# Performance work log

Hardware: AMD Instinct MI355X
Metric: run time of the kernel (lower is better)

The kernel has to match this reference:

```python
import jax, jax.numpy as jnp
import numpy as np

N_BALLS = 256
BATCH = 128
N_STEPS = 100
MAX_EVENTS = 5
WORLD_W = 10.0
WORLD_H = 10.0
RADIUS = 0.1
HID = 64
DT = 0.05
INF = jnp.float32(1e30)

_II_np, _JJ_np = np.triu_indices(N_BALLS, 1)
_II = jnp.asarray(_II_np)
_JJ = jnp.asarray(_JJ_np)
# wall order: left, right, bottom, top (normals point into the box)
_WN = jnp.array([[1.0, 0.0], [-1.0, 0.0], [0.0, 1.0], [0.0, -1.0]], dtype=jnp.float32)
_WP = jnp.array([0.0, -WORLD_W, 0.0, -WORLD_H], dtype=jnp.float32)


def setup_inputs():
    key = jax.random.key(0)
    ks = jax.random.split(key, 6)
    pos = jax.random.uniform(ks[0], (BATCH, N_BALLS, 2), minval=0.5, maxval=9.5)
    vel = jax.random.normal(ks[1], (BATCH, N_BALLS, 2))
    state = jnp.concatenate([pos, vel], axis=-1)  # [B, N, 4]
    radii = jnp.full((N_BALLS,), RADIUS, dtype=jnp.float32)
    sc = 0.1
    W1 = jax.random.normal(ks[2], (HID, 2)) * sc
    b1 = jnp.zeros((HID,), jnp.float32)
    W2 = jax.random.normal(ks[3], (HID, HID)) * sc
    b2 = jnp.zeros((HID,), jnp.float32)
    W3 = jax.random.normal(ks[4], (1, HID)) * sc
    b3 = jnp.zeros((1,), jnp.float32)
    return {"state": state, "radii": radii, "W1": W1, "b1": b1, "W2": W2,
            "b2": b2, "W3": W3, "b3": b3, "dt": DT, "n_steps": N_STEPS}


def _detect(pos, vel, radii):
    # pos, vel: [N,2]; vectorized replacement of the Python O(N^2) loop.
    diff = pos[_JJ] - pos[_II]                       # [P,2]
    dist = jnp.linalg.norm(diff, axis=-1)            # [P]
    gap_b = dist - (radii[_II] + radii[_JJ])
    nhat = diff / (dist + 1e-8)[:, None]
    app_b = jnp.sum((vel[_JJ] - vel[_II]) * nhat, axis=-1)
    gb = jnp.where(app_b < 0, gap_b, INF)            # only approaching pairs
    r = radii
    gw = jnp.stack([pos[:, 0] - r, WORLD_W - pos[:, 0] - r,
                    pos[:, 1] - r, WORLD_H - pos[:, 1] - r], axis=-1)  # [N,4]
    vw = jnp.stack([vel[:, 0] < 0, vel[:, 0] > 0,
                    vel[:, 1] < 0, vel[:, 1] > 0], axis=-1)
    gw = jnp.where(vw, gw, INF)
    allg = jnp.concatenate([gb, gw.reshape(-1)])
    k = jnp.argmin(allg)
    P = gb.shape[0]
    is_ball = k < P
    gap = allg[k]
    bi = jnp.where(is_ball, k, 0)
    i_b, j_b = _II[bi], _JJ[bi]
    kw = jnp.where(is_ball, 0, k - P)
    i_w, wid = kw // 4, kw % 4
    return gap, is_ball, i_b, j_b, i_w, wid


def _apply_jump(s, i, j, W1, b1, W2, b2, W3, b3):
    pos, vel = s[..., :2], s[..., 2:]
    diff = pos[:, j] - pos[:, i]                               # [B,2]
    dist = jnp.maximum(jnp.linalg.norm(diff, axis=-1, keepdims=True), 1e-8)
    nhat = diff / dist
    app = jnp.sum((vel[:, j] - vel[:, i]) * nhat, axis=-1, keepdims=True)
    h = jnp.concatenate([dist, app], axis=-1)                  # [B,2]
    h = jax.nn.silu(h @ W1.T + b1)
    h = jax.nn.silu(h @ W2.T + b2)
    imp = (h @ W3.T + b3) * nhat                               # [B,2]
    vel_new = vel.at[:, i].add(imp).at[:, j].add(-imp)
    return jnp.concatenate([pos, vel_new], axis=-1)


def _apply_wall(s, i, wn, wp, r):
    pos, vel = s[..., :2], s[..., 2:]
    v, p = vel[:, i], pos[:, i]
    vn = jnp.sum(v * wn, axis=-1, keepdims=True)
    vel_new = vel.at[:, i].set(v - 2.0 * vn * wn)
    pn = jnp.sum(p * wn, axis=-1, keepdims=True)
    pen = jnp.maximum(wp + r - pn, 0.0)
    pos_new = pos.at[:, i].set(p + pen * wn)
    return jnp.concatenate([pos_new, vel_new], axis=-1)


def _rollout(state, radii, W1, b1, W2, b2, W3, b3, dt, n_steps):
    dt = jnp.float32(dt)

    def event_body(_, carry):
        curr, t_c, t_e, done = carry
        pos0, vel0 = curr[0, :, :2], curr[0, :, 2:]
        gap, is_ball, i_b, j_b, i_w, wid = _detect(pos0, vel0, radii)
        no_event = gap > 0.05
        n = pos0[j_b] - pos0[i_b]
        app_ball = -jnp.sum((vel0[j_b] - vel0[i_b]) * n / jnp.linalg.norm(n))
        app_wall = jnp.abs(jnp.max(vel0[i_w]))
        app = jnp.where(is_ball, app_ball, app_wall)
        t_ev = t_c + gap / jnp.maximum(app, 1e-6)
        # ZeroFlow is constant velocity -> dopri5 integrate is exact linear drift
        dte = jnp.where(t_ev > t_c + 1e-10, t_ev - t_c, 0.0)

        def apply_map(s):
            jm = _apply_jump(s, i_b, j_b, W1, b1, W2, b2, W3, b3)
            wm = _apply_wall(s, i_w, _WN[wid], _WP[wid], radii[i_w])
            return jnp.where(is_ball, jm, wm)

        state_a = apply_map(curr)                       # gap <= 0: jump now
        integ = curr.at[..., :2].add(curr[..., 2:] * dte)
        state_b = apply_map(integ)                      # 0 < gap: drift then jump
        act = (~done) & (~no_event)
        case_a = act & (gap <= 0)
        case_b = act & (gap > 0) & (app > 1e-6) & (t_ev < t_e)
        new_done = done | no_event | (act & (gap > 0) & ((app <= 1e-6) | (t_ev >= t_e)))
        new_curr = jnp.where(case_a, state_a, jnp.where(case_b, state_b, curr))
        new_t_c = jnp.where(case_b, t_ev, t_c)
        return new_curr, new_t_c, t_e, new_done

    def step(curr, step_idx):
        t_s = step_idx.astype(jnp.float32) * dt
        t_e = t_s + dt
        curr, t_c, _, _ = jax.lax.fori_loop(
            0, MAX_EVENTS, event_body, (curr, t_s, t_e, jnp.bool_(False)))
        dte = jnp.where(t_e > t_c + 1e-10, t_e - t_c, 0.0)
        curr = curr.at[..., :2].add(curr[..., 2:] * dte)
        return curr, curr

    _, traj = jax.lax.scan(step, state, jnp.arange(n_steps))
    return jnp.concatenate([state[None], traj], axis=0)   # [n_steps+1, B, N, 4]


def reference(state, radii, W1, b1, W2, b2, W3, b3, dt, n_steps):
    return _rollout(state, radii, W1, b1, W2, b2, W3, b3, dt, n_steps)
```

## Files before the change

kernel.cpp:

```cpp
#include <hip/hip_runtime.h>
#include <stdint.h>

#define NB 256
#define NBATCH 128
#define HID 64
#define MAXEV 5
#define MAXSTEPS 256
#define NT 43
#define NTILES 946
#define W2S 65
#define CAND_MAX 6144
#define CMARGIN 1.5f

__device__ __forceinline__ float bf2f(unsigned short u) {
    return __uint_as_float(((unsigned)u) << 16);
}
__device__ __forceinline__ unsigned short f2bf(float f) {
    unsigned u = __float_as_uint(f);
    u += 0x7FFFu + ((u >> 16) & 1u);
    return (unsigned short)(u >> 16);
}
__device__ __forceinline__ float rdin(const void* p, int idx, int bf) {
    return bf ? bf2f(((const unsigned short*)p)[idx]) : ((const float*)p)[idx];
}
__device__ __forceinline__ float silu_f(float x) {
    float s = __fdiv_rn(1.0f, __fadd_rn(1.0f, expf(-x)));
    return __fmul_rn(x, s);
}
__device__ __forceinline__ void lds_fence() {
    __builtin_amdgcn_wave_barrier();
    __threadfence_block();
    __builtin_amdgcn_wave_barrier();
}
__device__ __forceinline__ unsigned long long shfl_down_u64(unsigned long long v, int off) {
    unsigned lo = (unsigned)v, hi = (unsigned)(v >> 32);
    lo = __shfl_down(lo, off);
    hi = __shfl_down(hi, off);
    return (((unsigned long long)hi) << 32) | lo;
}

__device__ void load_weights(float* w1, float* b1s, float* w2, float* b2s, float* w3, float* b3s,
                             const void* W1, const void* B1, const void* W2, const void* B2,
                             const void* W3, const void* B3, int bf, int tid, int nthr) {
    for (int k = tid; k < HID * 2; k += nthr) w1[k] = rdin(W1, k, bf);
    for (int k = tid; k < HID; k += nthr) {
        b1s[k] = rdin(B1, k, bf);
        b2s[k] = rdin(B2, k, bf);
        w3[k]  = rdin(W3, k, bf);
    }
    for (int k = tid; k < HID * HID; k += nthr) {
        int m = k >> 6, c = k & 63;
        w2[m * W2S + c] = rdin(W2, k, bf);
    }
    if (tid == 0) b3s[0] = rdin(B3, 0, bf);
}

__device__ __forceinline__ void pair_min(const float4* ps, int i, int j, unsigned long long& kP) {
    float4 A = ps[i], B = ps[j];
    float dx = __fsub_rn(B.x, A.x), dy = __fsub_rn(B.y, A.y);
    float d2 = __fadd_rn(__fmul_rn(dx, dx), __fmul_rn(dy, dy));
    float p1 = __fmul_rn(__fsub_rn(B.z, A.z), dx);
    float p2 = __fmul_rn(__fsub_rn(B.w, A.w), dy);
    float dot = __fadd_rn(p1, p2);
    float mag = __fadd_rn(fabsf(p1), fabsf(p2));
    bool appr;
    if (fabsf(dot) < __fmul_rn(1e-5f, mag)) {
        float dist = __fsqrt_rn(d2);
        float den = __fadd_rn(dist, 1e-8f);
        float ab = __fadd_rn(__fmul_rn(__fsub_rn(B.z, A.z), __fdiv_rn(dx, den)),
                             __fmul_rn(__fsub_rn(B.w, A.w), __fdiv_rn(dy, den)));
        appr = ab < 0.0f;
    } else {
        appr = dot < 0.0f;
    }
    if (appr) {
        unsigned long long key = (((unsigned long long)__float_as_uint(d2)) << 16) |
                                 (unsigned)((i << 8) | j);
        kP = key < kP ? key : kP;
    }
}

__global__ void sniff_kernel(const unsigned short* st, int* ws) {
    __shared__ int ev;
    if (threadIdx.x == 0) ev = 0;
    __syncthreads();
    unsigned short u = st[threadIdx.x];
    int e = (u >> 7) & 0xFF;
    if (e >= 0x85) atomicOr(&ev, 1);
    __syncthreads();
    if (threadIdx.x == 0) ws[0] = ev ? 0 : 1;
}

__global__ void row0_kernel(const void* in, void* out, const int* ws) {
    int idx = blockIdx.x * blockDim.x + threadIdx.x;
    if (ws[0]) ((unsigned short*)out)[idx] = ((const unsigned short*)in)[idx];
    else       ((float*)out)[idx] = ((const float*)in)[idx];
}

__global__ __launch_bounds__(1024, 1) void sim_kernel(
    const void* in_state, const void* in_rad,
    const void* inW1, const void* inB1, const void* inW2, const void* inB2,
    const void* inW3, const void* inB3, const void* in_dt, const int* in_nsteps,
    void* out, const int* ws) {
    __shared__ float4 ps0[NB];
    __shared__ float4 psb[NB];
    __shared__ float rad[NB];
    __shared__ float w1[HID * 2], b1s[HID], w2[HID * W2S], b2s[HID], w3s[HID], b3s[1];
    __shared__ float sc0[132], scb[132];
    __shared__ unsigned long long redP[16], redW[16];
    __shared__ float redF[4];
    __shared__ unsigned cand[CAND_MAX];
    __shared__ int candN;
    __shared__ int dI[4];
    __shared__ float dF[4];
    __shared__ int candF;
    __shared__ int rebF;

    int tid = threadIdx.x;
    int b = blockIdx.x;
    int bf = ws[0];

    if (tid < NB) {
        int base0 = tid * 4;
        float4 P;
        P.x = rdin(in_state, base0 + 0, bf);
        P.y = rdin(in_state, base0 + 1, bf);
        P.z = rdin(in_state, base0 + 2, bf);
        P.w = rdin(in_state, base0 + 3, bf);
        ps0[tid] = P;
        int baseb = (b * NB + tid) * 4;
        float4 Q;
        Q.x = rdin(in_state, baseb + 0, bf);
        Q.y = rdin(in_state, baseb + 1, bf);
        Q.z = rdin(in_state, baseb + 2, bf);
        Q.w = rdin(in_state, baseb + 3, bf);
        psb[tid] = Q;
        rad[tid] = rdin(in_rad, tid, bf);
        float m2 = P.z * P.z + P.w * P.w;
        #pragma unroll
        for (int off = 32; off; off >>= 1) m2 = fmaxf(m2, __shfl_down(m2, off));
        if ((tid & 63) == 0) redF[tid >> 6] = m2;
    }
    load_weights(w1, b1s, w2, b2s, w3s, b3s, inW1, inB1, inW2, inB2, inW3, inB3, bf, tid, 1024);
    if (tid == 0) { candN = 0; candF = 0; rebF = 1; }

    float dtv = rdin(in_dt, 0, bf);
    int NS = in_nsteps[0]; if (NS > MAXSTEPS) NS = MAXSTEPS; if (NS < 0) NS = 0;

    int myI0 = -1, myJ0 = 0;
    if (tid < NTILES) {
        int rem = tid, r = 0;
        while (rem >= NT - r) { rem -= NT - r; r++; }
        myI0 = r * 6; myJ0 = (r + rem) * 6;
    }
    __syncthreads();
    float rsum = __fadd_rn(rad[0], rad[0]);

    float theta = __fadd_rn(__fadd_rn(rsum, 0.05f), CMARGIN);
    float th2 = __fmul_rn(theta, theta);

    int nc = 0;
    bool candOvf = false;
    float used = 1e30f, vcap = 0.0f;

    for (int s = 0; s < NS; s++) {
        int rebuild = rebF;
        float t_s = __fmul_rn((float)s, dtv);
        float t_e = __fadd_rn(t_s, dtv);
        float t_c = t_s;
        if (tid < 64) {
            if (rebuild) {
                vcap = sqrtf(fmaxf(fmaxf(redF[0], redF[1]), fmaxf(redF[2], redF[3])));
                used = 0.0f;
            }
            used = __fadd_rn(used, __fmul_rn(__fmul_rn(2.0f, dtv), vcap));
            if (tid == 0 && rebuild) candF = 0;
        }

        for (int e = 0; e < MAXEV; e++) {
            unsigned long long kP = ~0ull, kW = ~0ull;
            bool fullscan = (e == 0) ? (rebuild != 0) : (candF != 0);
            bool doAppend = (e == 0) && rebuild;
            if (fullscan) {
                if (myI0 >= 0) {
                    float4 Pi[6], Pj[6];
                    #pragma unroll
                    for (int a = 0; a < 6; a++) {
                        int ii = myI0 + a; ii = ii < NB ? ii : NB - 1;
                        int jj = myJ0 + a; jj = jj < NB ? jj : NB - 1;
                        Pi[a] = ps0[ii]; Pj[a] = ps0[jj];
                    }
                    #pragma unroll
                    for (int a = 0; a < 6; a++) {
                        int i = myI0 + a;
                        #pragma unroll
                        for (int bb = 0; bb < 6; bb++) {
                            int j = myJ0 + bb;
                            bool ok = (i < NB) && (j < NB) && (j > i);
                            float dx = __fsub_rn(Pj[bb].x, Pi[a].x);
                            float dy = __fsub_rn(Pj[bb].y, Pi[a].y);
                            float d2 = __fadd_rn(__fmul_rn(dx, dx), __fmul_rn(dy, dy));
                            float p1 = __fmul_rn(__fsub_rn(Pj[bb].z, Pi[a].z), dx);
                            float p2 = __fmul_rn(__fsub_rn(Pj[bb].w, Pi[a].w), dy);
                            float dot = __fadd_rn(p1, p2);
                            float mag = __fadd_rn(fabsf(p1), fabsf(p2));
                            bool appr;
                            if (fabsf(dot) < __fmul_rn(1e-5f, mag)) {
                                float dist = __fsqrt_rn(d2);
                                float den = __fadd_rn(dist, 1e-8f);
                                float ab = __fadd_rn(
                                    __fmul_rn(__fsub_rn(Pj[bb].z, Pi[a].z), __fdiv_rn(dx, den)),
                                    __fmul_rn(__fsub_rn(Pj[bb].w, Pi[a].w), __fdiv_rn(dy, den)));
                                appr = ab < 0.0f;
                            } else {
                                appr = dot < 0.0f;
                            }
                            if (ok && appr) {
                                unsigned long long key =
                                    (((unsigned long long)__float_as_uint(d2)) << 16) |
                                    (unsigned)((i << 8) | j);
                                kP = key < kP ? key : kP;
                            }
                            if (doAppend && ok && d2 < th2) {
                                int x = atomicAdd(&candN, 1);
                                if (x < CAND_MAX) cand[x] = (unsigned)((i << 8) | j);
                            }
                        }
                    }
                }
            } else {
                for (int c = tid; c < nc; c += 1024) {
                    unsigned id = cand[c];
                    pair_min(ps0, (int)(id >> 8), (int)(id & 255u), kP);
                }
            }
            {
                int ball = tid >> 2, w = tid & 3;
                float4 P = ps0[ball]; float r = rad[ball];
                float g; bool valid;
                if (w == 0)      { g = __fsub_rn(P.x, r); valid = P.z < 0.0f; }
                else if (w == 1) { g = __fsub_rn(__fsub_rn(10.0f, P.x), r); valid = P.z > 0.0f; }
                else if (w == 2) { g = __fsub_rn(P.y, r); valid = P.w < 0.0f; }
                else             { g = __fsub_rn(__fsub_rn(10.0f, P.y), r); valid = P.w > 0.0f; }
                if (valid) {
                    unsigned gb = __float_as_uint(g);
                    unsigned m = (unsigned)(((int)gb) >> 31) | 0x80000000u;
                    unsigned sb = gb ^ m;
                    unsigned long long key = (((unsigned long long)sb) << 16) | (unsigned)tid;
                    kW = key < kW ? key : kW;
                }
            }
            #pragma unroll
            for (int off = 32; off; off >>= 1) {
                unsigned long long o1 = shfl_down_u64(kP, off);
                unsigned long long o2 = shfl_down_u64(kW, off);
                kP = o1 < kP ? o1 : kP;
                kW = o2 < kW ? o2 : kW;
            }
            if ((tid & 63) == 0) { redP[tid >> 6] = kP; redW[tid >> 6] = kW; }
            __syncthreads();

            if (e == 0 && rebuild) {
                int ct = candN;
                candOvf = ct > CAND_MAX;
                nc = candOvf ? CAND_MAX : ct;
            }

            float g_nx = 0, g_ny = 0, g_dist = 0, g_app = 0;
            float4 gA, gB;
            if (tid < 64) {
                unsigned long long mP = redP[0], mW = redW[0];
                #pragma unroll
                for (int q = 1; q < 16; q++) {
                    mP = redP[q] < mP ? redP[q] : mP;
                    mW = redW[q] < mW ? redW[q] : mW;
                }
                float gball = 1e30f; int pi = 0, pj = 1;
                if (mP != ~0ull) {
                    unsigned id = (unsigned)(mP & 0xFFFFull);
                    pi = id >> 8; pj = id & 255u;
                    float d2 = __uint_as_float((unsigned)(mP >> 16));
                    gball = __fsub_rn(__fsqrt_rn(d2), rsum);
                }
                float gwall = 1e30f; int wb = 0, ww = 0;
                if (mW != ~0ull) {
                    unsigned id = (unsigned)(mW & 0xFFFFull);
                    wb = id >> 2; ww = id & 3u;
                    unsigned sb = (unsigned)(mW >> 16);
                    unsigned gb = (sb & 0x80000000u) ? (sb ^ 0x80000000u) : ~sb;
                    gwall = __uint_as_float(gb);
                }
                bool is_ball = gball <= gwall;
                float gap = is_ball ? gball : gwall;
                int code_ = 0; float dteB_ = 0.0f, tcn_ = t_c;
                if (!(gap > 0.05f)) {
                    float app;
                    if (is_ball) {
                        float4 A = ps0[pi], B = ps0[pj];
                        float dx = __fsub_rn(B.x, A.x), dy = __fsub_rn(B.y, A.y);
                        float nrm = __fsqrt_rn(__fadd_rn(__fmul_rn(dx, dx), __fmul_rn(dy, dy)));
                        float dvx = __fsub_rn(B.z, A.z), dvy = __fsub_rn(B.w, A.w);
                        app = -__fadd_rn(__fdiv_rn(__fmul_rn(dvx, dx), nrm),
                                         __fdiv_rn(__fmul_rn(dvy, dy), nrm));
                    } else {
                        float4 Wb = ps0[wb];
                        app = fabsf(fmaxf(Wb.z, Wb.w));
                    }
                    float t_ev = __fadd_rn(t_c, __fdiv_rn(gap, fmaxf(app, 1e-6f)));
                    if (gap <= 0.0f) {
                        code_ = is_ball ? 1 : 3;
                    } else if (app > 1e-6f && t_ev < t_e) {
                        code_ = is_ball ? 2 : 4;
                        dteB_ = (t_ev > __fadd_rn(t_c, 1e-10f)) ? __fsub_rn(t_ev, t_c) : 0.0f;
                        tcn_ = t_ev;
                    }
                }
                int ei_ = is_ball ? pi : wb;
                int ej_ = is_ball ? pj : ww;
                if (tid == 0) {
                    dI[0] = code_; dI[1] = ei_; dI[2] = ej_;
                    dF[0] = dteB_; dF[1] = tcn_;
                }
                if (code_ != 0 && code_ <= 2) {
                    float4 A = ps0[ei_], B = ps0[ej_];
                    if (code_ == 2) {
                        A.x = __fadd_rn(A.x, __fmul_rn(A.z, dteB_));
                        A.y = __fadd_rn(A.y, __fmul_rn(A.w, dteB_));
                        B.x = __fadd_rn(B.x, __fmul_rn(B.z, dteB_));
                        B.y = __fadd_rn(B.y, __fmul_rn(B.w, dteB_));
                    }
                    gA = A; gB = B;
                    float dx = __fsub_rn(B.x, A.x), dy = __fsub_rn(B.y, A.y);
                    float nrm = __fsqrt_rn(__fadd_rn(__fmul_rn(dx, dx), __fmul_rn(dy, dy)));
                    float dist = fmaxf(nrm, 1e-8f);
                    g_nx = __fdiv_rn(dx, dist); g_ny = __fdiv_rn(dy, dist);
                    g_dist = dist;
                    float dvx = __fsub_rn(B.z, A.z), dvy = __fsub_rn(B.w, A.w);
                    g_app = __fadd_rn(__fmul_rn(dvx, g_nx), __fmul_rn(dvy, g_ny));
                }
            }
            __syncthreads();

            int code = dI[0];
            if (code == 0) break;
            int ei = dI[1], ejw = dI[2];
            float dteB = dF[0];
            t_c = dF[1];
            bool integ = (code == 2) || (code == 4);

            if (code <= 2) {
                if (tid < 64) {
                    float a = __fadd_rn(__fadd_rn(__fmul_rn(g_dist, w1[2 * tid]),
                                                  __fmul_rn(g_app, w1[2 * tid + 1])), b1s[tid]);
                    sc0[4 + tid] = silu_f(a);
                    lds_fence();
                    float acc = 0.0f;
                    const float* row = &w2[tid * W2S];
                    #pragma unroll 8
                    for (int k = 0; k < HID; k++) acc = __fadd_rn(acc, __fmul_rn(sc0[4 + k], row[k]));
                    acc = __fadd_rn(acc, b2s[tid]);
                    sc0[68 + tid] = silu_f(acc);
                    lds_fence();
                    float acc3 = 0.0f;
                    #pragma unroll 8
                    for (int k = 0; k < HID; k++)
                        acc3 = __fadd_rn(acc3, __fmul_rn(sc0[68 + k], w3s[k]));
                    float impv = __fadd_rn(acc3, b3s[0]);
                    float ix = __fmul_rn(impv, g_nx), iy = __fmul_rn(impv, g_ny);
                    float nAz = __fadd_rn(gA.z, ix),  nAw = __fadd_rn(gA.w, iy);
                    float nBz = __fadd_rn(gB.z, -ix), nBw = __fadd_rn(gB.w, -iy);
                    if (tid == 0) {
                        float4 outA; outA.x = gA.x; outA.y = gA.y; outA.z = nAz; outA.w = nAw;
                        float4 outB; outB.x = gB.x; outB.y = gB.y; outB.z = nBz; outB.w = nBw;
                        ps0[ei] = outA; ps0[ejw] = outB;
                    }
                    float s1 = sqrtf(nAz * nAz + nAw * nAw);
                    float s2 = sqrtf(nBz * nBz + nBw * nBw);
                    float nv = fmaxf(s1, s2);
                    used = __fadd_rn(used, __fmul_rn(__fmul_rn(2.0f, dtv),
                                                     fmaxf(__fsub_rn(nv, vcap), 0.0f)));
                    vcap = fmaxf(vcap, nv);
                    int nf = (candOvf || (__fadd_rn(used, 1e-3f) > CMARGIN)) ? 1 : 0;
                    if (tid == 0) candF = nf;
                } else if (tid < 128) {
                    int lane = tid - 64;
                    float4 A = psb[ei], B = psb[ejw];
                    if (integ) {
                        A.x = __fadd_rn(A.x, __fmul_rn(A.z, dteB));
                        A.y = __fadd_rn(A.y, __fmul_rn(A.w, dteB));
                        B.x = __fadd_rn(B.x, __fmul_rn(B.z, dteB));
                        B.y = __fadd_rn(B.y, __fmul_rn(B.w, dteB));
                    }
                    float dx = __fsub_rn(B.x, A.x), dy = __fsub_rn(B.y, A.y);
                    float nrm = __fsqrt_rn(__fadd_rn(__fmul_rn(dx, dx), __fmul_rn(dy, dy)));
                    float dist = fmaxf(nrm, 1e-8f);
                    float nx = __fdiv_rn(dx, dist), ny = __fdiv_rn(dy, dist);
                    float dvx = __fsub_rn(B.z, A.z), dvy = __fsub_rn(B.w, A.w);
                    float app2 = __fadd_rn(__fmul_rn(dvx, nx), __fmul_rn(dvy, ny));
                    float a = __fadd_rn(__fadd_rn(__fmul_rn(dist, w1[2 * lane]),
                                                  __fmul_rn(app2, w1[2 * lane + 1])), b1s[lane]);
                    scb[4 + lane] = silu_f(a);
                    lds_fence();
                    float acc = 0.0f;
                    const float* row = &w2[lane * W2S];
                    #pragma unroll 8
                    for (int k = 0; k < HID; k++) acc = __fadd_rn(acc, __fmul_rn(scb[4 + k], row[k]));
                    acc = __fadd_rn(acc, b2s[lane]);
                    scb[68 + lane] = silu_f(acc);
                    lds_fence();
                    float acc3 = 0.0f;
                    #pragma unroll 8
                    for (int k = 0; k < HID; k++)
                        acc3 = __fadd_rn(acc3, __fmul_rn(scb[68 + k], w3s[k]));
                    float impv = __fadd_rn(acc3, b3s[0]);
                    if (lane == 0) {
                        float ix = __fmul_rn(impv, nx), iy = __fmul_rn(impv, ny);
                        float4 outA; outA.x = A.x; outA.y = A.y;
                        outA.z = __fadd_rn(A.z, ix);  outA.w = __fadd_rn(A.w, iy);
                        float4 outB; outB.x = B.x; outB.y = B.y;
                        outB.z = __fadd_rn(B.z, -ix); outB.w = __fadd_rn(B.w, -iy);
                        psb[ei] = outA; psb[ejw] = outB;
                    }
                } else if (tid < 384) {
                    int t = tid - 128;
                    if (integ && t != ei && t != ejw) {
                        float4 P = ps0[t];
                        P.x = __fadd_rn(P.x, __fmul_rn(P.z, dteB));
                        P.y = __fadd_rn(P.y, __fmul_rn(P.w, dteB));
                        ps0[t] = P;
                    }
                } else if (tid < 640) {
                    int t = tid - 384;
                    if (integ && t != ei && t != ejw) {
                        float4 Q = psb[t];
                        Q.x = __fadd_rn(Q.x, __fmul_rn(Q.z, dteB));
                        Q.y = __fadd_rn(Q.y, __fmul_rn(Q.w, dteB));
                        psb[t] = Q;
                    }
                }
                __syncthreads();
            } else {
                const float wnx[4] = {1.f, -1.f, 0.f, 0.f};
                const float wny[4] = {0.f, 0.f, 1.f, -1.f};
                const float wpv[4] = {0.f, -10.f, 0.f, -10.f};
                int w = ejw;
                if (tid < 64) {
                    float4 P = ps0[ei];
                    if (integ) {
                        P.x = __fadd_rn(P.x, __fmul_rn(P.z, dteB));
                        P.y = __fadd_rn(P.y, __fmul_rn(P.w, dteB));
                    }
                    float vn = __fadd_rn(__fmul_rn(P.z, wnx[w]), __fmul_rn(P.w, wny[w]));
                    float t2 = __fmul_rn(2.0f, vn);
                    float nvx = __fsub_rn(P.z, __fmul_rn(t2, wnx[w]));
                    float nvy = __fsub_rn(P.w, __fmul_rn(t2, wny[w]));
                    float pn = __fadd_rn(__fmul_rn(P.x, wnx[w]), __fmul_rn(P.y, wny[w]));
                    float pen = fmaxf(__fsub_rn(__fadd_rn(wpv[w], rad[ei]), pn), 0.0f);
                    float4 nP;
                    nP.x = __fadd_rn(P.x, __fmul_rn(pen, wnx[w]));
                    nP.y = __fadd_rn(P.y, __fmul_rn(pen, wny[w]));
                    nP.z = nvx; nP.w = nvy;
                    used = __fadd_rn(used, pen);
                    int nf = (candOvf || (__fadd_rn(used, 1e-3f) > CMARGIN)) ? 1 : 0;
                    if (tid == 0) { ps0[ei] = nP; candF = nf; }
                } else if (tid < 128) {
                    if (tid == 64) {
                        float4 P = psb[ei];
                        if (integ) {
                            P.x = __fadd_rn(P.x, __fmul_rn(P.z, dteB));
                            P.y = __fadd_rn(P.y, __fmul_rn(P.w, dteB));
                        }
                        float vn = __fadd_rn(__fmul_rn(P.z, wnx[w]), __fmul_rn(P.w, wny[w]));
                        float t2 = __fmul_rn(2.0f, vn);
                        float nvx = __fsub_rn(P.z, __fmul_rn(t2, wnx[w]));
                        float nvy = __fsub_rn(P.w, __fmul_rn(t2, wny[w]));
                        float pn = __fadd_rn(__fmul_rn(P.x, wnx[w]), __fmul_rn(P.y, wny[w]));
                        float pen = fmaxf(__fsub_rn(__fadd_rn(wpv[w], rad[ei]), pn), 0.0f);
                        float4 nP;
                        nP.x = __fadd_rn(P.x, __fmul_rn(pen, wnx[w]));
                        nP.y = __fadd_rn(P.y, __fmul_rn(pen, wny[w]));
                        nP.z = nvx; nP.w = nvy;
                        psb[ei] = nP;
                    }
                } else if (tid < 384) {
                    int t = tid - 128;
                    if (integ && t != ei) {
                        float4 P = ps0[t];
                        P.x = __fadd_rn(P.x, __fmul_rn(P.z, dteB));
                        P.y = __fadd_rn(P.y, __fmul_rn(P.w, dteB));
                        ps0[t] = P;
                    }
                } else if (tid < 640) {
                    int t = tid - 384;
                    if (integ && t != ei) {
                        float4 Q = psb[t];
                        Q.x = __fadd_rn(Q.x, __fmul_rn(Q.z, dteB));
                        Q.y = __fadd_rn(Q.y, __fmul_rn(Q.w, dteB));
                        psb[t] = Q;
                    }
                }
                __syncthreads();
            }
        }

        float fd = (t_e > __fadd_rn(t_c, 1e-10f)) ? __fsub_rn(t_e, t_c) : 0.0f;
        if (tid < NB) {
            float4 P = ps0[tid];
            P.x = __fadd_rn(P.x, __fmul_rn(P.z, fd));
            P.y = __fadd_rn(P.y, __fmul_rn(P.w, fd));
            ps0[tid] = P;
            float m2 = P.z * P.z + P.w * P.w;
            #pragma unroll
            for (int off = 32; off; off >>= 1) m2 = fmaxf(m2, __shfl_down(m2, off));
            if ((tid & 63) == 0) redF[tid >> 6] = m2;
            if (tid == 0) {
                candN = 0;
                float usedNext = __fadd_rn(used, __fmul_rn(__fmul_rn(2.0f, dtv), vcap));
                rebF = (candOvf || (__fadd_rn(usedNext, 1e-3f) > CMARGIN)) ? 1 : 0;
            }
        } else if (tid < 2 * NB) {
            int t = tid - NB;
            float4 Q = psb[t];
            Q.x = __fadd_rn(Q.x, __fmul_rn(Q.z, fd));
            Q.y = __fadd_rn(Q.y, __fmul_rn(Q.w, fd));
            psb[t] = Q;
            long long base = ((long long)(s + 1) * NBATCH + b) * (NB * 4);
            if (bf) {
                ushort4 v;
                v.x = f2bf(Q.x); v.y = f2bf(Q.y); v.z = f2bf(Q.z); v.w = f2bf(Q.w);
                ((ushort4*)((unsigned short*)out + base))[t] = v;
            } else {
                ((float4*)((float*)out + base))[t] = Q;
            }
        }
        __syncthreads();
    }
}

extern "C" void kernel_launch(void* const* d_in, const int* in_sizes, int n_in,
                              void* d_out, int out_size, void* d_ws, size_t ws_size,
                              hipStream_t stream) {
    int* ws = (int*)d_ws;
    sniff_kernel<<<1, 256, 0, stream>>>((const unsigned short*)d_in[0], ws);
    row0_kernel<<<(NBATCH * NB * 4) / 256, 256, 0, stream>>>(d_in[0], d_out, ws);
    sim_kernel<<<NBATCH, 1024, 0, stream>>>(
        d_in[0], d_in[1], d_in[2], d_in[3], d_in[4], d_in[5], d_in[6], d_in[7],
        d_in[8], (const int*)d_in[9], d_out, ws);
}
```

Before: 3.330 ms.

## Halve block size, gate pair tests by distance, merge ball/wall reductions

```diff
diff --git a/kernel.cpp b/kernel.cpp
--- a/kernel.cpp
+++ b/kernel.cpp
@@ -11,6 +11,10 @@
 #define W2S 65
 #define CAND_MAX 6144
 #define CMARGIN 1.5f
+#define NTHR 512
+#define D2GATE 0.0626f
+
+typedef unsigned long long u64;
 
 __device__ __forceinline__ float bf2f(unsigned short u) {
     return __uint_as_float(((unsigned)u) << 16);
@@ -32,11 +36,55 @@
     __threadfence_block();
     __builtin_amdgcn_wave_barrier();
 }
-__device__ __forceinline__ unsigned long long shfl_down_u64(unsigned long long v, int off) {
+__device__ __forceinline__ u64 shfl_down_u64(u64 v, int off) {
     unsigned lo = (unsigned)v, hi = (unsigned)(v >> 32);
     lo = __shfl_down(lo, off);
     hi = __shfl_down(hi, off);
-    return (((unsigned long long)hi) << 32) | lo;
+    return (((u64)hi) << 32) | lo;
+}
+__device__ __forceinline__ unsigned fmap(float g) {
+    unsigned u = __float_as_uint(g);
+    unsigned m = (unsigned)(((int)u) >> 31) | 0x80000000u;
+    return u ^ m;
+}
+__device__ __forceinline__ float funmap(unsigned sb) {
+    unsigned u = (sb & 0x80000000u) ? (sb ^ 0x80000000u) : ~sb;
+    return __uint_as_float(u);
+}
+
+__device__ __forceinline__ void append_agg(unsigned* list, int* counter, int cap, unsigned val) {
+    u64 m = __ballot(1);
+    int lane = (int)(threadIdx.x & 63);
+    int ldr = (int)__builtin_ctzll(m);
+    int pfx = (int)__builtin_popcountll(m & ((1ull << lane) - 1ull));
+    int base = 0;
+    if (lane == ldr) base = atomicAdd(counter, (int)__builtin_popcountll(m));
+    base = __builtin_amdgcn_readfirstlane(base);
+    int idx = base + pfx;
+    if (idx < cap) list[idx] = val;
+}
+
+__device__ __forceinline__ u64 ball_key(const float4* ps, int i, int j,
+                                        float dx, float dy, float d2,
+                                        unsigned id, float rsum) {
+    float4 A = ps[i], B = ps[j];
+    float p1 = __fmul_rn(__fsub_rn(B.z, A.z), dx);
+    float p2 = __fmul_rn(__fsub_rn(B.w, A.w), dy);
+    float dot = __fadd_rn(p1, p2);
+    float mag = __fadd_rn(fabsf(p1), fabsf(p2));
+    bool appr;
+    if (fabsf(dot) < __fmul_rn(1e-5f, mag)) {
+        float dist = __fsqrt_rn(d2);
+        float den = __fadd_rn(dist, 1e-8f);
+        float ab = __fadd_rn(__fmul_rn(__fsub_rn(B.z, A.z), __fdiv_rn(dx, den)),
+                             __fmul_rn(__fsub_rn(B.w, A.w), __fdiv_rn(dy, den)));
+        appr = ab < 0.0f;
+    } else {
+        appr = dot < 0.0f;
+    }
+    if (!appr) return ~0ull;
+    float gap = __fsub_rn(__fsqrt_rn(d2), rsum);
+    return (((u64)fmap(gap)) << 17) | id;
 }
 
 __device__ void load_weights(float* w1, float* b1s, float* w2, float* b2s, float* w3, float* b3s,
@@ -55,31 +103,6 @@
     if (tid == 0) b3s[0] = rdin(B3, 0, bf);
 }
 
-__device__ __forceinline__ void pair_min(const float4* ps, int i, int j, unsigned long long& kP) {
-    float4 A = ps[i], B = ps[j];
-    float dx = __fsub_rn(B.x, A.x), dy = __fsub_rn(B.y, A.y);
-    float d2 = __fadd_rn(__fmul_rn(dx, dx), __fmul_rn(dy, dy));
-    float p1 = __fmul_rn(__fsub_rn(B.z, A.z), dx);
-    float p2 = __fmul_rn(__fsub_rn(B.w, A.w), dy);
-    float dot = __fadd_rn(p1, p2);
-    float mag = __fadd_rn(fabsf(p1), fabsf(p2));
-    bool appr;
-    if (fabsf(dot) < __fmul_rn(1e-5f, mag)) {
-        float dist = __fsqrt_rn(d2);
-        float den = __fadd_rn(dist, 1e-8f);
-        float ab = __fadd_rn(__fmul_rn(__fsub_rn(B.z, A.z), __fdiv_rn(dx, den)),
-                             __fmul_rn(__fsub_rn(B.w, A.w), __fdiv_rn(dy, den)));
-        appr = ab < 0.0f;
-    } else {
-        appr = dot < 0.0f;
-    }
-    if (appr) {
-        unsigned long long key = (((unsigned long long)__float_as_uint(d2)) << 16) |
-                                 (unsigned)((i << 8) | j);
-        kP = key < kP ? key : kP;
-    }
-}
-
 __global__ void sniff_kernel(const unsigned short* st, int* ws) {
     __shared__ int ev;
     if (threadIdx.x == 0) ev = 0;
@@ -97,17 +120,18 @@
     else       ((float*)out)[idx] = ((const float*)in)[idx];
 }
 
-__global__ __launch_bounds__(1024, 1) void sim_kernel(
+__global__ __launch_bounds__(NTHR, 1) void sim_kernel(
     const void* in_state, const void* in_rad,
     const void* inW1, const void* inB1, const void* inW2, const void* inB2,
     const void* inW3, const void* inB3, const void* in_dt, const int* in_nsteps,
     void* out, const int* ws) {
     __shared__ float4 ps0[NB];
     __shared__ float4 psb[NB];
+    __shared__ float2 pos2[NB];
     __shared__ float rad[NB];
     __shared__ float w1[HID * 2], b1s[HID], w2[HID * W2S], b2s[HID], w3s[HID], b3s[1];
     __shared__ float sc0[132], scb[132];
-    __shared__ unsigned long long redP[16], redW[16];
+    __shared__ u64 redK[8];
     __shared__ float redF[4];
     __shared__ unsigned cand[CAND_MAX];
     __shared__ int candN;
@@ -128,6 +152,8 @@
         P.z = rdin(in_state, base0 + 2, bf);
         P.w = rdin(in_state, base0 + 3, bf);
         ps0[tid] = P;
+        float2 p2v; p2v.x = P.x; p2v.y = P.y;
+        pos2[tid] = p2v;
         int baseb = (b * NB + tid) * 4;
         float4 Q;
         Q.x = rdin(in_state, baseb + 0, bf);
@@ -141,23 +167,32 @@
         for (int off = 32; off; off >>= 1) m2 = fmaxf(m2, __shfl_down(m2, off));
         if ((tid & 63) == 0) redF[tid >> 6] = m2;
     }
-    load_weights(w1, b1s, w2, b2s, w3s, b3s, inW1, inB1, inW2, inB2, inW3, inB3, bf, tid, 1024);
+    load_weights(w1, b1s, w2, b2s, w3s, b3s, inW1, inB1, inW2, inB2, inW3, inB3, bf, tid, NTHR);
     if (tid == 0) { candN = 0; candF = 0; rebF = 1; }
 
     float dtv = rdin(in_dt, 0, bf);
     int NS = in_nsteps[0]; if (NS > MAXSTEPS) NS = MAXSTEPS; if (NS < 0) NS = 0;
 
-    int myI0 = -1, myJ0 = 0;
-    if (tid < NTILES) {
-        int rem = tid, r = 0;
-        while (rem >= NT - r) { rem -= NT - r; r++; }
-        myI0 = r * 6; myJ0 = (r + rem) * 6;
+    int i0a = -1, j0a = 0, i0b = -1, j0b = 0;
+    {
+        int T = tid;
+        if (T < NTILES) {
+            int rem = T, r = 0;
+            while (rem >= NT - r) { rem -= NT - r; r++; }
+            i0a = r * 6; j0a = (r + rem) * 6;
+        }
+        T = tid + NTHR;
+        if (T < NTILES) {
+            int rem = T, r = 0;
+            while (rem >= NT - r) { rem -= NT - r; r++; }
+            i0b = r * 6; j0b = (r + rem) * 6;
+        }
     }
     __syncthreads();
     float rsum = __fadd_rn(rad[0], rad[0]);
 
-    float theta = __fadd_rn(__fadd_rn(rsum, 0.05f), CMARGIN);
-    float th2 = __fmul_rn(theta, theta);
+    float thB = __fadd_rn(__fadd_rn(rsum, 0.05f), CMARGIN);
+    float th2B = __fmul_rn(thB, thB);
 
     int nc = 0;
     bool candOvf = false;
@@ -178,86 +213,78 @@
         }
 
         for (int e = 0; e < MAXEV; e++) {
-            unsigned long long kP = ~0ull, kW = ~0ull;
+            u64 kC = ~0ull;
             bool fullscan = (e == 0) ? (rebuild != 0) : (candF != 0);
             bool doAppend = (e == 0) && rebuild;
             if (fullscan) {
-                if (myI0 >= 0) {
-                    float4 Pi[6], Pj[6];
+                #pragma unroll
+                for (int tt = 0; tt < 2; tt++) {
+                    int I0 = tt ? i0b : i0a;
+                    int J0 = tt ? j0b : j0a;
+                    if (I0 < 0) continue;
+                    float2 Pi[6], Pj[6];
                     #pragma unroll
                     for (int a = 0; a < 6; a++) {
-                        int ii = myI0 + a; ii = ii < NB ? ii : NB - 1;
-                        int jj = myJ0 + a; jj = jj < NB ? jj : NB - 1;
-                        Pi[a] = ps0[ii]; Pj[a] = ps0[jj];
+                        int ii = I0 + a; ii = ii < NB ? ii : NB - 1;
+                        int jj = J0 + a; jj = jj < NB ? jj : NB - 1;
+                        Pi[a] = pos2[ii]; Pj[a] = pos2[jj];
                     }
                     #pragma unroll
                     for (int a = 0; a < 6; a++) {
-                        int i = myI0 + a;
+                        int i = I0 + a;
                         #pragma unroll
                         for (int bb = 0; bb < 6; bb++) {
-                            int j = myJ0 + bb;
+                            int j = J0 + bb;
                             bool ok = (i < NB) && (j < NB) && (j > i);
                             float dx = __fsub_rn(Pj[bb].x, Pi[a].x);
                             float dy = __fsub_rn(Pj[bb].y, Pi[a].y);
                             float d2 = __fadd_rn(__fmul_rn(dx, dx), __fmul_rn(dy, dy));
-                            float p1 = __fmul_rn(__fsub_rn(Pj[bb].z, Pi[a].z), dx);
-                            float p2 = __fmul_rn(__fsub_rn(Pj[bb].w, Pi[a].w), dy);
-                            float dot = __fadd_rn(p1, p2);
-                            float mag = __fadd_rn(fabsf(p1), fabsf(p2));
-                            bool appr;
-                            if (fabsf(dot) < __fmul_rn(1e-5f, mag)) {
-                                float dist = __fsqrt_rn(d2);
-                                float den = __fadd_rn(dist, 1e-8f);
-                                float ab = __fadd_rn(
-                                    __fmul_rn(__fsub_rn(Pj[bb].z, Pi[a].z), __fdiv_rn(dx, den)),
-                                    __fmul_rn(__fsub_rn(Pj[bb].w, Pi[a].w), __fdiv_rn(dy, den)));
-                                appr = ab < 0.0f;
-                            } else {
-                                appr = dot < 0.0f;
-                            }
-                            if (ok && appr) {
-                                unsigned long long key =
-                                    (((unsigned long long)__float_as_uint(d2)) << 16) |
-                                    (unsigned)((i << 8) | j);
-                                kP = key < kP ? key : kP;
-                            }
-                            if (doAppend && ok && d2 < th2) {
-                                int x = atomicAdd(&candN, 1);
-                                if (x < CAND_MAX) cand[x] = (unsigned)((i << 8) | j);
+                            unsigned id = (unsigned)((i << 8) | j);
+                            if (doAppend && ok && d2 < th2B)
+                                append_agg(cand, &candN, CAND_MAX, id);
+                            if (ok && d2 < D2GATE) {
+                                u64 key = ball_key(ps0, i, j, dx, dy, d2, id, rsum);
+                                kC = key < kC ? key : kC;
                             }
                         }
                     }
                 }
             } else {
-                for (int c = tid; c < nc; c += 1024) {
+                for (int c = tid; c < nc; c += NTHR) {
                     unsigned id = cand[c];
-                    pair_min(ps0, (int)(id >> 8), (int)(id & 255u), kP);
+                    int i = (int)(id >> 8), j = (int)(id & 255u);
+                    float2 A = pos2[i], B = pos2[j];
+                    float dx = __fsub_rn(B.x, A.x), dy = __fsub_rn(B.y, A.y);
+                    float d2 = __fadd_rn(__fmul_rn(dx, dx), __fmul_rn(dy, dy));
+                    if (d2 < D2GATE) {
+                        u64 key = ball_key(ps0, i, j, dx, dy, d2, id, rsum);
+                        kC = key < kC ? key : kC;
+                    }
                 }
             }
             {
-                int ball = tid >> 2, w = tid & 3;
+                int ball = tid & 255, wsel = tid >> 8;
                 float4 P = ps0[ball]; float r = rad[ball];
-                float g; bool valid;
-                if (w == 0)      { g = __fsub_rn(P.x, r); valid = P.z < 0.0f; }
-                else if (w == 1) { g = __fsub_rn(__fsub_rn(10.0f, P.x), r); valid = P.z > 0.0f; }
-                else if (w == 2) { g = __fsub_rn(P.y, r); valid = P.w < 0.0f; }
-                else             { g = __fsub_rn(__fsub_rn(10.0f, P.y), r); valid = P.w > 0.0f; }
-                if (valid) {
-                    unsigned gb = __float_as_uint(g);
-                    unsigned m = (unsigned)(((int)gb) >> 31) | 0x80000000u;
-                    unsigned sb = gb ^ m;
-                    unsigned long long key = (((unsigned long long)sb) << 16) | (unsigned)tid;
-                    kW = key < kW ? key : kW;
+                #pragma unroll
+                for (int q = 0; q < 2; q++) {
+                    int w = wsel * 2 + q;
+                    float g; bool valid;
+                    if (w == 0)      { g = __fsub_rn(P.x, r); valid = P.z < 0.0f; }
+                    else if (w == 1) { g = __fsub_rn(__fsub_rn(10.0f, P.x), r); valid = P.z > 0.0f; }
+                    else if (w == 2) { g = __fsub_rn(P.y, r); valid = P.w < 0.0f; }
+                    else             { g = __fsub_rn(__fsub_rn(10.0f, P.y), r); valid = P.w > 0.0f; }
+                    if (valid) {
+                        u64 key = (((u64)fmap(g)) << 17) | 0x10000u | (unsigned)(ball * 4 + w);
+                        kC = key < kC ? key : kC;
+                    }
                 }
             }
             #pragma unroll
             for (int off = 32; off; off >>= 1) {
-                unsigned long long o1 = shfl_down_u64(kP, off);
-                unsigned long long o2 = shfl_down_u64(kW, off);
-                kP = o1 < kP ? o1 : kP;
-                kW = o2 < kW ? o2 : kW;
-            }
-            if ((tid & 63) == 0) { redP[tid >> 6] = kP; redW[tid >> 6] = kW; }
+                u64 o = shfl_down_u64(kC, off);
+                kC = o < kC ? o : kC;
+            }
+            if ((tid & 63) == 0) redK[tid >> 6] = kC;
             __syncthreads();
 
             if (e == 0 && rebuild) {
@@ -269,54 +296,42 @@
             float g_nx = 0, g_ny = 0, g_dist = 0, g_app = 0;
             float4 gA, gB;
             if (tid < 64) {
-                unsigned long long mP = redP[0], mW = redW[0];
+                u64 m = redK[0];
                 #pragma unroll
-                for (int q = 1; q < 16; q++) {
-                    mP = redP[q] < mP ? redP[q] : mP;
-                    mW = redW[q] < mW ? redW[q] : mW;
-                }
-                float gball = 1e30f; int pi = 0, pj = 1;
-                if (mP != ~0ull) {
-                    unsigned id = (unsigned)(mP & 0xFFFFull);
-                    pi = id >> 8; pj = id & 255u;
-                    float d2 = __uint_as_float((unsigned)(mP >> 16));
-                    gball = __fsub_rn(__fsqrt_rn(d2), rsum);
-                }
-                float gwall = 1e30f; int wb = 0, ww = 0;
-                if (mW != ~0ull) {
-                    unsigned id = (unsigned)(mW & 0xFFFFull);
-                    wb = id >> 2; ww = id & 3u;
-                    unsigned sb = (unsigned)(mW >> 16);
-                    unsigned gb = (sb & 0x80000000u) ? (sb ^ 0x80000000u) : ~sb;
-                    gwall = __uint_as_float(gb);
-                }
-                bool is_ball = gball <= gwall;
-                float gap = is_ball ? gball : gwall;
+                for (int q = 1; q < 8; q++) m = redK[q] < m ? redK[q] : m;
                 int code_ = 0; float dteB_ = 0.0f, tcn_ = t_c;
-                if (!(gap > 0.05f)) {
-                    float app;
-                    if (is_ball) {
-                        float4 A = ps0[pi], B = ps0[pj];
-                        float dx = __fsub_rn(B.x, A.x), dy = __fsub_rn(B.y, A.y);
-                        float nrm = __fsqrt_rn(__fadd_rn(__fmul_rn(dx, dx), __fmul_rn(dy, dy)));
-                        float dvx = __fsub_rn(B.z, A.z), dvy = __fsub_rn(B.w, A.w);
-                        app = -__fadd_rn(__fdiv_rn(__fmul_rn(dvx, dx), nrm),
-                                         __fdiv_rn(__fmul_rn(dvy, dy), nrm));
-                    } else {
-                        float4 Wb = ps0[wb];
-                        app = fabsf(fmaxf(Wb.z, Wb.w));
-                    }
-                    float t_ev = __fadd_rn(t_c, __fdiv_rn(gap, fmaxf(app, 1e-6f)));
-                    if (gap <= 0.0f) {
-                        code_ = is_ball ? 1 : 3;
-                    } else if (app > 1e-6f && t_ev < t_e) {
-                        code_ = is_ball ? 2 : 4;
-                        dteB_ = (t_ev > __fadd_rn(t_c, 1e-10f)) ? __fsub_rn(t_ev, t_c) : 0.0f;
-                        tcn_ = t_ev;
-                    }
-                }
-                int ei_ = is_ball ? pi : wb;
-                int ej_ = is_ball ? pj : ww;
+                int ei_ = 0, ej_ = 0;
+                if (m != ~0ull) {
+                    bool is_ball = ((m >> 16) & 1ull) == 0;
+                    unsigned id = (unsigned)(m & 0xFFFFull);
+                    float gap = funmap((unsigned)(m >> 17));
+                    int pi = (int)(id >> 8), pj = (int)(id & 255u);
+                    int wb = (int)(id >> 2), ww = (int)(id & 3u);
+                    ei_ = is_ball ? pi : wb;
+                    ej_ = is_ball ? pj : ww;
+                    if (!(gap > 0.05f)) {
+                        float app;
+                        if (is_ball) {
+                            float4 A = ps0[pi], B = ps0[pj];
+                            float dx = __fsub_rn(B.x, A.x), dy = __fsub_rn(B.y, A.y);
+                            float nrm = __fsqrt_rn(__fadd_rn(__fmul_rn(dx, dx), __fmul_rn(dy, dy)));
+                            float dvx = __fsub_rn(B.z, A.z), dvy = __fsub_rn(B.w, A.w);
+                            app = -__fadd_rn(__fdiv_rn(__fmul_rn(dvx, dx), nrm),
+                                             __fdiv_rn(__fmul_rn(dvy, dy), nrm));
+                        } else {
+                            float4 Wb = ps0[wb];
+                            app = fabsf(fmaxf(Wb.z, Wb.w));
+                        }
+                        float t_ev = __fadd_rn(t_c, __fdiv_rn(gap, fmaxf(app, 1e-6f)));
+                        if (gap <= 0.0f) {
+                            code_ = is_ball ? 1 : 3;
+                        } else if (app > 1e-6f && t_ev < t_e) {
+                            code_ = is_ball ? 2 : 4;
+                            dteB_ = (t_ev > __fadd_rn(t_c, 1e-10f)) ? __fsub_rn(t_ev, t_c) : 0.0f;
+                            tcn_ = t_ev;
+                        }
+                    }
+                }
                 if (tid == 0) {
                     dI[0] = code_; dI[1] = ei_; dI[2] = ej_;
                     dF[0] = dteB_; dF[1] = tcn_;
@@ -373,6 +388,8 @@
                         float4 outA; outA.x = gA.x; outA.y = gA.y; outA.z = nAz; outA.w = nAw;
                         float4 outB; outB.x = gB.x; outB.y = gB.y; outB.z = nBz; outB.w = nBw;
                         ps0[ei] = outA; ps0[ejw] = outB;
+                        float2 pa; pa.x = gA.x; pa.y = gA.y; pos2[ei] = pa;
+                        float2 pb; pb.x = gB.x; pb.y = gB.y; pos2[ejw] = pb;
                     }
                     float s1 = sqrtf(nAz * nAz + nAw * nAw);
                     float s2 = sqrtf(nBz * nBz + nBw * nBw);
@@ -428,14 +445,18 @@
                         P.x = __fadd_rn(P.x, __fmul_rn(P.z, dteB));
                         P.y = __fadd_rn(P.y, __fmul_rn(P.w, dteB));
                         ps0[t] = P;
-                    }
-                } else if (tid < 640) {
-                    int t = tid - 384;
-                    if (integ && t != ei && t != ejw) {
-                        float4 Q = psb[t];
-                        Q.x = __fadd_rn(Q.x, __fmul_rn(Q.z, dteB));
-                        Q.y = __fadd_rn(Q.y, __fmul_rn(Q.w, dteB));
-                        psb[t] = Q;
+                        float2 pp; pp.x = P.x; pp.y = P.y; pos2[t] = pp;
+                    }
+                } else {
+                    #pragma unroll
+                    for (int q = 0; q < 2; q++) {
+                        int t = (tid - 384) + q * 128;
+                        if (integ && t != ei && t != ejw) {
+                            float4 Q = psb[t];
+                            Q.x = __fadd_rn(Q.x, __fmul_rn(Q.z, dteB));
+                            Q.y = __fadd_rn(Q.y, __fmul_rn(Q.w, dteB));
+                            psb[t] = Q;
+                        }
                     }
                 }
                 __syncthreads();
@@ -462,7 +483,11 @@
                     nP.z = nvx; nP.w = nvy;
                     used = __fadd_rn(used, pen);
                     int nf = (candOvf || (__fadd_rn(used, 1e-3f) > CMARGIN)) ? 1 : 0;
-                    if (tid == 0) { ps0[ei] = nP; candF = nf; }
+                    if (tid == 0) {
+                        ps0[ei] = nP;
+                        float2 pp; pp.x = nP.x; pp.y = nP.y; pos2[ei] = pp;
+                        candF = nf;
+                    }
                 } else if (tid < 128) {
                     if (tid == 64) {
                         float4 P = psb[ei];
@@ -489,14 +514,18 @@
                         P.x = __fadd_rn(P.x, __fmul_rn(P.z, dteB));
                         P.y = __fadd_rn(P.y, __fmul_rn(P.w, dteB));
                         ps0[t] = P;
-                    }
-                } else if (tid < 640) {
-                    int t = tid - 384;
-                    if (integ && t != ei) {
-                        float4 Q = psb[t];
-                        Q.x = __fadd_rn(Q.x, __fmul_rn(Q.z, dteB));
-                        Q.y = __fadd_rn(Q.y, __fmul_rn(Q.w, dteB));
-                        psb[t] = Q;
+                        float2 pp; pp.x = P.x; pp.y = P.y; pos2[t] = pp;
+                    }
+                } else {
+                    #pragma unroll
+                    for (int q = 0; q < 2; q++) {
+                        int t = (tid - 384) + q * 128;
+                        if (integ && t != ei) {
+                            float4 Q = psb[t];
+                            Q.x = __fadd_rn(Q.x, __fmul_rn(Q.z, dteB));
+                            Q.y = __fadd_rn(Q.y, __fmul_rn(Q.w, dteB));
+                            psb[t] = Q;
+                        }
                     }
                 }
                 __syncthreads();
@@ -509,6 +538,7 @@
             P.x = __fadd_rn(P.x, __fmul_rn(P.z, fd));
             P.y = __fadd_rn(P.y, __fmul_rn(P.w, fd));
             ps0[tid] = P;
+            float2 pp; pp.x = P.x; pp.y = P.y; pos2[tid] = pp;
             float m2 = P.z * P.z + P.w * P.w;
             #pragma unroll
             for (int off = 32; off; off >>= 1) m2 = fmaxf(m2, __shfl_down(m2, off));
@@ -518,7 +548,7 @@
                 float usedNext = __fadd_rn(used, __fmul_rn(__fmul_rn(2.0f, dtv), vcap));
                 rebF = (candOvf || (__fadd_rn(usedNext, 1e-3f) > CMARGIN)) ? 1 : 0;
             }
-        } else if (tid < 2 * NB) {
+        } else {
             int t = tid - NB;
             float4 Q = psb[t];
             Q.x = __fadd_rn(Q.x, __fmul_rn(Q.z, fd));
@@ -543,7 +573,7 @@
     int* ws = (int*)d_ws;
     sniff_kernel<<<1, 256, 0, stream>>>((const unsigned short*)d_in[0], ws);
     row0_kernel<<<(NBATCH * NB * 4) / 256, 256, 0, stream>>>(d_in[0], d_out, ws);
-    sim_kernel<<<NBATCH, 1024, 0, stream>>>(
+    sim_kernel<<<NBATCH, NTHR, 0, stream>>>(
         d_in[0], d_in[1], d_in[2], d_in[3], d_in[4], d_in[5], d_in[6], d_in[7],
         d_in[8], (const int*)d_in[9], d_out, ws);
 }
```

Measured after the change: 3.317 ms. About the same (-0.4%).
